# Kernel tuning notes

Hardware: AMD Instinct MI355X
Metric: run time of the kernel (lower is better)

Reference implementation:

```python
import jax, jax.numpy as jnp
import numpy as np

B = 131072
FLOW_SIZE = 16
PASS = 8
TRANS = FLOW_SIZE - PASS  # 8
N_BINS = 128
HIDDEN = 256


def setup_inputs() -> dict:
    key = jax.random.key(0)
    k0, k1, k2 = jax.random.split(key, 3)
    x = jax.random.uniform(k0, (B, FLOW_SIZE + 1), dtype=jnp.float32)
    W1 = jax.random.normal(k1, (PASS, HIDDEN), dtype=jnp.float32) * 0.3
    b1 = jnp.zeros((HIDDEN,), dtype=jnp.float32)
    W2 = jax.random.normal(k2, (HIDDEN, TRANS * N_BINS), dtype=jnp.float32) * 0.05
    b2 = jnp.zeros((TRANS * N_BINS,), dtype=jnp.float32)
    return {"x": x, "W1": W1, "b1": b1, "W2": W2, "b2": b2}


def reference(x, W1, b1, W2, b2):
    xA = x[:, :PASS]                      # [B, P]
    xB = x[:, PASS:FLOW_SIZE]             # [B, T]
    jacobian = x[:, FLOW_SIZE:FLOW_SIZE + 1]  # [B, 1]

    # NN: small MLP, exp output -> positive unnormalized bin widths Q [B, T, n_bins]
    h = jax.nn.relu(xA @ W1 + b1)
    Q = jnp.exp(h @ W2 + b2).reshape(x.shape[0], TRANS, N_BINS)

    Qsum = jnp.cumsum(Q, axis=-1)                     # [B, T, n_bins]
    Qnorms = Qsum[:, :, -1:]                          # [B, T, 1]
    Q = Q / (Qnorms / N_BINS)                         # normalized slopes
    Qsum = Qsum / Qnorms                              # normalized CDF
    Qsum = jnp.pad(Qsum, ((0, 0), (0, 0), (1, 0)))    # left-pad CDF with 0

    alphas = xB * N_BINS
    bins = jnp.floor(alphas)
    alphas = (alphas - bins) / N_BINS                 # fractional offset within bin
    bins = jnp.clip(bins.astype(jnp.int32), 0, N_BINS - 1)

    cdf_int_part = jnp.take_along_axis(Qsum, bins[..., None], axis=-1)[..., 0]  # [B, T]
    cdf_float_part = jnp.take_along_axis(Q, bins[..., None], axis=-1)[..., 0]   # [B, T]

    cdf = cdf_float_part * alphas + cdf_int_part      # [B, T]
    jacobian = jacobian * jnp.prod(cdf_float_part, axis=-1, keepdims=True)  # [B, 1]

    return jnp.concatenate((xA, cdf, jacobian), axis=-1)  # [B, flow_size+1]
```

## Files before the change

### kernel.cpp

```cpp
#include <hip/hip_runtime.h>
#include <math.h>

#define NROWS 131072
#define XC    17
#define ROWSB 64
#define HID   256
#define NB    128
#define NCOL  1024
#define LOG2E 1.44269504088896340736f

typedef __attribute__((ext_vector_type(8))) short bf16x8;
typedef __attribute__((ext_vector_type(4))) float f32x4;

#if __has_builtin(__builtin_amdgcn_exp2f)
#define EXP2F(v) __builtin_amdgcn_exp2f(v)
#else
#define EXP2F(v) exp2f(v)
#endif
#if __has_builtin(__builtin_amdgcn_rcpf)
#define RCPF(v) __builtin_amdgcn_rcpf(v)
#else
#define RCPF(v) (1.f / (v))
#endif

__device__ __forceinline__ unsigned short f2bf(float f) {
    unsigned int u = __float_as_uint(f);
    return (unsigned short)((u + 0x7FFFu + ((u >> 16) & 1u)) >> 16);
}

__device__ __forceinline__ float red16(float v) {
    int x;
    x = __builtin_amdgcn_update_dpp(0, __float_as_int(v), 0xB1, 0xF, 0xF, true);
    v += __int_as_float(x);
    x = __builtin_amdgcn_update_dpp(0, __float_as_int(v), 0x4E, 0xF, 0xF, true);
    v += __int_as_float(x);
    x = __builtin_amdgcn_update_dpp(0, __float_as_int(v), 0x141, 0xF, 0xF, true);
    v += __int_as_float(x);
    x = __builtin_amdgcn_update_dpp(0, __float_as_int(v), 0x140, 0xF, 0xF, true);
    v += __int_as_float(x);
    return v;
}

__global__ void prep_w2(const float* __restrict__ W2, unsigned short* __restrict__ w2t) {
    __shared__ __align__(16) unsigned short tkT[32][80];
    const int tid = threadIdx.x;
    const int k0 = (blockIdx.x & 3) * 64;
    const int c0 = (blockIdx.x >> 2) * 32;
    const int c4 = (tid & 7) * 4;
    const int kk = (tid >> 3) * 2;
    const float4 r0 = *(const float4*)&W2[(size_t)(k0 + kk) * NCOL + c0 + c4];
    const float4 r1 = *(const float4*)&W2[(size_t)(k0 + kk + 1) * NCOL + c0 + c4];
    const float v0[4] = {r0.x, r0.y, r0.z, r0.w};
    const float v1[4] = {r1.x, r1.y, r1.z, r1.w};
    #pragma unroll
    for (int i = 0; i < 4; ++i) {
        const unsigned int p = (unsigned int)f2bf(v0[i] * LOG2E)
                             | ((unsigned int)f2bf(v1[i] * LOG2E) << 16);
        *(unsigned int*)&tkT[c4 + i][kk] = p;
    }
    __syncthreads();
    const int g = tid & 7, c = tid >> 3;
    const uint4 q = *(const uint4*)&tkT[c][g * 8];
    *(uint4*)&w2t[(size_t)(c0 + c) * HID + k0 + ((g ^ (c & 7)) << 3)] = q;
}

__global__ __launch_bounds__(256, 4)
void gplc6(const float* __restrict__ x,
           const float* __restrict__ W1,
           const float* __restrict__ b1,
           const unsigned short* __restrict__ w2t,
           const float* __restrict__ b2,
           float* __restrict__ out)
{
    __shared__ float xs[ROWSB * XC];
    __shared__ __align__(16) union {
        unsigned short hb[32 * HID];
        unsigned short w2[2][64 * 64];
    } u;

    const int tid  = threadIdx.x;
    const int lane = tid & 63;
    const int w    = tid >> 6;
    const int quad = lane >> 4;
    const int l15  = lane & 15;
    const int wr   = w * 16;
    const int ksw  = (lane & 7) << 3;
    const size_t r0 = (size_t)blockIdx.x * ROWSB;

    for (int i = tid; i < ROWSB * XC; i += 256) xs[i] = x[r0 * XC + i];
    const int cp = tid & 127, hlf = tid >> 7;
    float w1r[16];
    #pragma unroll
    for (int i = 0; i < 8; ++i) {
        const float2 t2 = *(const float2*)&W1[i * HID + 2 * cp];
        w1r[2 * i] = t2.x; w1r[2 * i + 1] = t2.y;
    }
    const float2 b1v = *(const float2*)&b1[2 * cp];
    __syncthreads();

    bf16x8 afr[8];
    #pragma unroll
    for (int ch = 0; ch < 2; ++ch) {
        for (int r = 0; r < 16; ++r) {
            const int lrow = hlf * 16 + r;
            const int row  = ch * 32 + lrow;
            float a0 = b1v.x, a1 = b1v.y;
            #pragma unroll
            for (int i = 0; i < 8; ++i) {
                const float xv = xs[row * XC + i];
                a0 = fmaf(xv, w1r[2 * i], a0);
                a1 = fmaf(xv, w1r[2 * i + 1], a1);
            }
            a0 = fmaxf(a0, 0.f); a1 = fmaxf(a1, 0.f);
            const int eidx = lrow * HID + (((cp >> 2) ^ (row & 15)) << 3) + ((cp & 3) << 1);
            *(unsigned int*)&u.hb[eidx] = (unsigned int)f2bf(a0) | ((unsigned int)f2bf(a1) << 16);
        }
        __syncthreads();
        if ((w >> 1) == ch) {
            #pragma unroll
            for (int kf = 0; kf < 8; ++kf) {
                const int row = wr + l15;
                afr[kf] = *(const bf16x8*)&u.hb[(row & 31) * HID + (((kf * 4 + quad) ^ l15) << 3)];
            }
        }
        __syncthreads();
    }

    auto stage = [&](int m) {
        const int t = m >> 3, cj = (m >> 2) & 1, kc = m & 3, buf = m & 1;
        #pragma unroll
        for (int j = 0; j < 2; ++j) {
            const int ci  = (w * 2 + j) * 8 + (lane >> 3);
            const int col = t * NB + cj * 64 + ci;
            const int kl  = (lane & 7) << 3;
            const unsigned short* gp = w2t + (size_t)col * HID + kc * 64 + kl;
            unsigned short* lp = &u.w2[buf][(w * 2 + j) * 512];
            __builtin_amdgcn_global_load_lds(
                (const __attribute__((address_space(1))) unsigned int*)gp,
                (__attribute__((address_space(3))) unsigned int*)lp, 16, 0, 0);
        }
    };

    float jf[4] = {1.f, 1.f, 1.f, 1.f};

    stage(0);
    #pragma unroll 1
    for (int t = 0; t < 8; ++t) {
        f32x4 acc[8];
        #pragma unroll
        for (int ct = 0; ct < 8; ++ct) acc[ct] = (f32x4){0.f, 0.f, 0.f, 0.f};

        #pragma unroll
        for (int cj = 0; cj < 2; ++cj) {
            #pragma unroll
            for (int kc = 0; kc < 4; ++kc) {
                __syncthreads();
                const int m = t * 8 + cj * 4 + kc;
                if (m < 63) stage(m + 1);
                const unsigned short* wsb = u.w2[m & 1];
                #pragma unroll
                for (int ks = 0; ks < 2; ++ks) {
                    const int kf = kc * 2 + ks;
                    const int klog = ks * 32 + quad * 8;
                    #pragma unroll
                    for (int ci = 0; ci < 4; ++ci) {
                        const int ct = cj * 4 + ci;
                        const int c  = ci * 16 + l15;
                        const bf16x8 bf = *(const bf16x8*)&wsb[c * 64 + (klog ^ ksw)];
                        acc[ct] = __builtin_amdgcn_mfma_f32_16x16x32_bf16(afr[kf], bf, acc[ct], 0, 0, 0);
                    }
                }
            }
        }

        #pragma unroll
        for (int ct = 0; ct < 8; ++ct) {
            const float bbv = b2[t * NB + ct * 16 + l15] * LOG2E;
            acc[ct][0] += bbv; acc[ct][1] += bbv; acc[ct][2] += bbv; acc[ct][3] += bbv;
        }

        #pragma unroll
        for (int i = 0; i < 4; ++i) {
            const int row = wr + quad * 4 + i;
            const float alpha = xs[row * XC + 8 + t] * 128.f;
            const float fb = floorf(alpha);
            const int bin = min(max((int)fb, 0), 127);
            const float fr = alpha - fb;
            float e[8];
            #pragma unroll
            for (int ct = 0; ct < 8; ++ct) e[ct] = EXP2F(acc[ct][i]);
            const float P1 = e[0],      P2 = P1 + e[1], P3 = P2 + e[2], P4 = P3 + e[3];
            const float P5 = P4 + e[4], P6 = P5 + e[5], P7 = P6 + e[6], P8 = P7 + e[7];
            int thr = (bin - l15 + 15) >> 4;
            thr = min(max(thr, 0), 8);
            const float sA = (thr & 1) ? P1 : 0.f;
            const float sB = (thr & 1) ? P3 : P2;
            const float sC = (thr & 1) ? P5 : P4;
            const float sD = (thr & 1) ? P7 : P6;
            const float sE = (thr & 2) ? sB : sA;
            const float sF = (thr & 2) ? sD : sC;
            float num = (thr & 4) ? sF : sE;
            num = (thr >= 8) ? P8 : num;
            const int cb = bin >> 4;
            const float t1 = (cb & 1) ? e[1] : e[0];
            const float t2 = (cb & 1) ? e[3] : e[2];
            const float t3 = (cb & 1) ? e[5] : e[4];
            const float t4 = (cb & 1) ? e[7] : e[6];
            const float u1 = (cb & 2) ? t2 : t1;
            const float u2 = (cb & 2) ? t4 : t3;
            const float es = (cb & 4) ? u2 : u1;
            float eb  = ((bin & 15) == l15) ? es : 0.f;
            float tot = P8;
            tot = red16(tot); num = red16(num); eb = red16(eb);
            const float inv = RCPF(tot);
            jf[i] *= 128.f * eb * inv;
            if (l15 == 0) xs[row * XC + 8 + t] = fmaf(eb, fr, num) * inv;
        }
    }

    if (l15 == 0) {
        #pragma unroll
        for (int i = 0; i < 4; ++i) {
            const int row = wr + quad * 4 + i;
            xs[row * XC + 16] *= jf[i];
        }
    }
    __syncthreads();
    for (int i = tid; i < ROWSB * XC; i += 256) out[r0 * XC + i] = xs[i];
}

extern "C" void kernel_launch(void* const* d_in, const int* in_sizes, int n_in,
                              void* d_out, int out_size, void* d_ws, size_t ws_size,
                              hipStream_t stream) {
    (void)in_sizes; (void)n_in; (void)ws_size; (void)out_size;
    prep_w2<<<128, 256, 0, stream>>>((const float*)d_in[3], (unsigned short*)d_ws);
    gplc6<<<NROWS / ROWSB, 256, 0, stream>>>(
        (const float*)d_in[0], (const float*)d_in[1], (const float*)d_in[2],
        (const unsigned short*)d_ws, (const float*)d_in[4], (float*)d_out);
}
```

Measured before the change: 169.5 us.

## Deepen W2 LDS pipeline to four buffers with explicit vmcnt waits

Moves the W2 tile staging from a double buffer to a four-slot ring with three tiles in flight. The full __syncthreads per k-chunk is replaced by counted s_waitcnt vmcnt waits plus s_barrier, and the MFMA section runs at raised wave priority. The bias b2 is preloaded once into LDS as bf16 (pre-scaled by log2e) and added just before exp2 instead of being read from global memory every tile. This adds LDS use, which can lower occupancy, and rounding the bias to bf16 adds error, which is zero here since the test bias is all zeros. The hand-set wait counts are fragile if the number of loads per stage ever changes.

```diff
diff --git a/kernel.cpp b/kernel.cpp
--- a/kernel.cpp
+++ b/kernel.cpp
@@ -75,7 +75,10 @@
     __shared__ float xs[ROWSB * XC];
     __shared__ __align__(16) union {
         unsigned short hb[32 * HID];
-        unsigned short w2[2][64 * 64];
+        struct {
+            unsigned short w2[4][64 * 64];
+            unsigned short b2s[NCOL];
+        } g;
     } u;
 
     const int tid  = threadIdx.x;
@@ -126,15 +129,19 @@
         __syncthreads();
     }
 
+    for (int i = tid; i < NCOL; i += 256) u.g.b2s[i] = f2bf(b2[i] * LOG2E);
+    asm volatile("s_waitcnt lgkmcnt(0)" ::: "memory");
+    __builtin_amdgcn_sched_barrier(0);
+
     auto stage = [&](int m) {
-        const int t = m >> 3, cj = (m >> 2) & 1, kc = m & 3, buf = m & 1;
+        const int t = m >> 3, cj = (m >> 2) & 1, buf = m & 3;
         #pragma unroll
         for (int j = 0; j < 2; ++j) {
             const int ci  = (w * 2 + j) * 8 + (lane >> 3);
             const int col = t * NB + cj * 64 + ci;
             const int kl  = (lane & 7) << 3;
-            const unsigned short* gp = w2t + (size_t)col * HID + kc * 64 + kl;
-            unsigned short* lp = &u.w2[buf][(w * 2 + j) * 512];
+            const unsigned short* gp = w2t + (size_t)col * HID + buf * 64 + kl;
+            unsigned short* lp = &u.g.w2[buf][(w * 2 + j) * 512];
             __builtin_amdgcn_global_load_lds(
                 (const __attribute__((address_space(1))) unsigned int*)gp,
                 (__attribute__((address_space(3))) unsigned int*)lp, 16, 0, 0);
@@ -143,7 +150,7 @@
 
     float jf[4] = {1.f, 1.f, 1.f, 1.f};
 
-    stage(0);
+    stage(0); stage(1); stage(2);
     #pragma unroll 1
     for (int t = 0; t < 8; ++t) {
         f32x4 acc[8];
@@ -154,10 +161,21 @@
         for (int cj = 0; cj < 2; ++cj) {
             #pragma unroll
             for (int kc = 0; kc < 4; ++kc) {
-                __syncthreads();
                 const int m = t * 8 + cj * 4 + kc;
-                if (m < 63) stage(m + 1);
-                const unsigned short* wsb = u.w2[m & 1];
+                if (cj == 1 && kc == 2) {
+                    if (t == 7) { asm volatile("s_waitcnt vmcnt(2)" ::: "memory"); }
+                    else        { asm volatile("s_waitcnt vmcnt(4)" ::: "memory"); }
+                } else if (cj == 1 && kc == 3) {
+                    if (t == 7) { asm volatile("s_waitcnt vmcnt(0)" ::: "memory"); }
+                    else        { asm volatile("s_waitcnt vmcnt(4)" ::: "memory"); }
+                } else {
+                    asm volatile("s_waitcnt vmcnt(4)" ::: "memory");
+                }
+                __builtin_amdgcn_s_barrier();
+                if (m <= 60) stage(m + 3);
+
+                __builtin_amdgcn_s_setprio(1);
+                const unsigned short* wsb = u.g.w2[kc];
                 #pragma unroll
                 for (int ks = 0; ks < 2; ++ks) {
                     const int kf = kc * 2 + ks;
@@ -170,15 +188,14 @@
                         acc[ct] = __builtin_amdgcn_mfma_f32_16x16x32_bf16(afr[kf], bf, acc[ct], 0, 0, 0);
                     }
                 }
+                __builtin_amdgcn_s_setprio(0);
             }
         }
 
-        #pragma unroll
-        for (int ct = 0; ct < 8; ++ct) {
-            const float bbv = b2[t * NB + ct * 16 + l15] * LOG2E;
-            acc[ct][0] += bbv; acc[ct][1] += bbv; acc[ct][2] += bbv; acc[ct][3] += bbv;
-        }
-
+        float bb[8];
+        #pragma unroll
+        for (int ct = 0; ct < 8; ++ct)
+            bb[ct] = __uint_as_float((unsigned int)u.g.b2s[t * NB + ct * 16 + l15] << 16);
         #pragma unroll
         for (int i = 0; i < 4; ++i) {
             const int row = wr + quad * 4 + i;
@@ -188,7 +205,7 @@
             const float fr = alpha - fb;
             float e[8];
             #pragma unroll
-            for (int ct = 0; ct < 8; ++ct) e[ct] = EXP2F(acc[ct][i]);
+            for (int ct = 0; ct < 8; ++ct) e[ct] = EXP2F(acc[ct][i] + bb[ct]);
             const float P1 = e[0],      P2 = P1 + e[1], P3 = P2 + e[2], P4 = P3 + e[3];
             const float P5 = P4 + e[4], P6 = P5 + e[5], P7 = P6 + e[6], P8 = P7 + e[7];
             int thr = (bin - l15 + 15) >> 4;
```

Result: no change. 168.4 us (-0.7%).
